# Optimization experiments

Measured on AMD Instinct MI355X. Metric: run time of the kernel, lower is better.

The kernel has to match this reference:

```python
import jax, jax.numpy as jnp
import numpy as np

B, G, C = 16384, 7, 30  # batch, 7x7 grid, 2*5 box params + 20 classes


def setup_inputs() -> dict:
    key = jax.random.key(0)
    k1, k2 = jax.random.split(key)
    pred = jax.random.uniform(k1, (B, G, G, C), dtype=jnp.float32)
    labels = jax.random.uniform(k2, (B, G, G, C), dtype=jnp.float32)
    # channel 0 of labels is the object-presence indicator (==1 where a gt box exists)
    labels = labels.at[..., 0].set((labels[..., 0] > 0.7).astype(jnp.float32))
    return {"pred": pred, "labels": labels}


def _corners(box):
    # box channels: [conf, x, y, w, h]
    x, y, w, h = box[..., 1], box[..., 2], box[..., 3], box[..., 4]
    return x - 0.5 * w, x + 0.5 * w, y - 0.5 * h, y + 0.5 * h  # left,right,top,bottom


def _iou(b1, b2):
    l1, r1, t1, bt1 = _corners(b1)
    l2, r2, t2, bt2 = _corners(b2)
    in_h = jnp.minimum(bt1, bt2) - jnp.maximum(t1, t2)
    in_w = jnp.minimum(r1, r2) - jnp.maximum(l1, l2)
    inter = jnp.where((in_h < 0) | (in_w < 0), 0.0, in_h * in_w)
    area1 = (bt1 - t1) * (r1 - l1)
    area2 = (bt2 - t2) * (r2 - l2)
    return inter / (area1 + area2 - inter)


def reference(pred, labels):
    mask = labels[..., 0]                     # [B,7,7] object indicator (0/1)
    box1 = pred[..., 0:5]
    box2 = pred[..., 5:10]
    gt = labels[..., 0:5]
    iou1 = _iou(box1, gt)
    iou2 = _iou(box2, gt)
    best = iou1 >= iou2                       # responsible box per cell
    sel = jnp.where(best[..., None], box1, box2)
    iou_max = jnp.where(best, iou1, iou2)
    iou_min = jnp.where(best, iou2, iou1)
    center = 5.0 * ((sel[..., 1] - gt[..., 1]) ** 2 + (sel[..., 2] - gt[..., 2]) ** 2)
    wh = 5.0 * ((jnp.sqrt(sel[..., 3]) - jnp.sqrt(gt[..., 3])) ** 2
                + (jnp.sqrt(sel[..., 4]) - jnp.sqrt(gt[..., 4])) ** 2)
    cls = jnp.sum((pred[..., 10:] - labels[..., 10:]) ** 2, axis=-1)

    def msum(x):
        return jnp.sum(x * mask)

    # [center, wh, obj_conf, noobj_conf, classification]
    return jnp.stack([msum(center), msum(wh), msum(iou_max), msum(iou_min), msum(cls)])
```

## Files before the change

### kernel.cpp

```cpp
#include <hip/hip_runtime.h>

#define NCH 30
#define TPB 256

typedef float v4f __attribute__((ext_vector_type(4)));
typedef float v2f __attribute__((ext_vector_type(2)));

__device__ __forceinline__ float iou_f(float x1, float y1, float w1, float h1,
                                       float x2, float y2, float w2, float h2) {
    float l1 = x1 - 0.5f * w1, r1 = x1 + 0.5f * w1;
    float t1 = y1 - 0.5f * h1, b1 = y1 + 0.5f * h1;
    float l2 = x2 - 0.5f * w2, r2 = x2 + 0.5f * w2;
    float t2 = y2 - 0.5f * h2, b2 = y2 + 0.5f * h2;
    float in_h = fminf(b1, b2) - fmaxf(t1, t2);
    float in_w = fminf(r1, r2) - fmaxf(l1, l2);
    float inter = (in_h < 0.f || in_w < 0.f) ? 0.f : in_h * in_w;
    float a1 = (b1 - t1) * (r1 - l1);
    float a2 = (b2 - t2) * (r2 - l2);
    return inter / (a1 + a2 - inter);
}

#define PF(i) (P[(i) >> 2][(i) & 3])
#define LF(i) (L[(i) >> 2][(i) & 3])

__device__ __forceinline__ void cell_terms(const v4f* P, const v4f* L, int o, float mask,
                                           float& v0, float& v1, float& v2,
                                           float& v3, float& v4) {
    const float gx = LF(o + 1), gy = LF(o + 2), gw = LF(o + 3), gh = LF(o + 4);
    const float i1 = iou_f(PF(o + 1), PF(o + 2), PF(o + 3), PF(o + 4), gx, gy, gw, gh);
    const float i2 = iou_f(PF(o + 6), PF(o + 7), PF(o + 8), PF(o + 9), gx, gy, gw, gh);
    const bool best = (i1 >= i2);
    const float sx = best ? PF(o + 1) : PF(o + 6);
    const float sy = best ? PF(o + 2) : PF(o + 7);
    const float sw = best ? PF(o + 3) : PF(o + 8);
    const float sh = best ? PF(o + 4) : PF(o + 9);
    const float imax = best ? i1 : i2;
    const float imin = best ? i2 : i1;

    const float center = 5.f * ((sx - gx) * (sx - gx) + (sy - gy) * (sy - gy));
    const float dw = sqrtf(sw) - sqrtf(gw);
    const float dh = sqrtf(sh) - sqrtf(gh);
    const float wh = 5.f * (dw * dw + dh * dh);

    float cls = 0.f;
#pragma unroll
    for (int c = 10; c < 30; ++c) {
        const float d = PF(o + c) - LF(o + c);
        cls += d * d;
    }

    v0 += center * mask;
    v1 += wh * mask;
    v2 += imax * mask;
    v3 += imin * mask;
    v4 += cls * mask;
}

__global__ __launch_bounds__(TPB) void yolo_partial(const float* __restrict__ pred,
                                                    const float* __restrict__ lab,
                                                    float* __restrict__ partial,
                                                    int n_pairs) {
    __shared__ float red[5][TPB / 64];
    const int tid = threadIdx.x;
    const size_t p = (size_t)blockIdx.x * TPB + tid;

    float v0 = 0.f, v1 = 0.f, v2 = 0.f, v3 = 0.f, v4 = 0.f;

    if (p < (size_t)n_pairs) {
        const float* lp = lab + p * (2 * NCH);
        const v2f mA = *(const v2f*)(lp);
        const v2f mB = *(const v2f*)(lp + NCH);
        const float maskA = mA[0], maskB = mB[0];

        if (maskA != 0.f || maskB != 0.f) {
            const float* pp = pred + p * (2 * NCH);
            v4f P[15], L[15];
#pragma unroll
            for (int k = 0; k < 15; ++k) P[k] = *(const v4f*)(pp + 4 * k);
#pragma unroll
            for (int k = 0; k < 15; ++k) L[k] = *(const v4f*)(lp + 4 * k);

            if (maskA != 0.f) cell_terms(P, L, 0,   maskA, v0, v1, v2, v3, v4);
            if (maskB != 0.f) cell_terms(P, L, NCH, maskB, v0, v1, v2, v3, v4);
        }
    }

#pragma unroll
    for (int off = 32; off > 0; off >>= 1) {
        v0 += __shfl_down(v0, off);
        v1 += __shfl_down(v1, off);
        v2 += __shfl_down(v2, off);
        v3 += __shfl_down(v3, off);
        v4 += __shfl_down(v4, off);
    }

    const int wave = tid >> 6;
    const int lane = tid & 63;
    if (lane == 0) {
        red[0][wave] = v0;
        red[1][wave] = v1;
        red[2][wave] = v2;
        red[3][wave] = v3;
        red[4][wave] = v4;
    }
    __syncthreads();

    if (tid < 5) {
        float s = 0.f;
#pragma unroll
        for (int w = 0; w < TPB / 64; ++w) s += red[tid][w];
        partial[(size_t)blockIdx.x * 5 + tid] = s;
    }
}

__global__ __launch_bounds__(256) void final_reduce(const float* __restrict__ partial,
                                                    float* __restrict__ out,
                                                    int n_blocks) {
    __shared__ float red[5][4];
    const int tid = threadIdx.x;
    float v0 = 0.f, v1 = 0.f, v2 = 0.f, v3 = 0.f, v4 = 0.f;
    for (int b = tid; b < n_blocks; b += 256) {
        const float* q = partial + (size_t)b * 5;
        v0 += q[0]; v1 += q[1]; v2 += q[2]; v3 += q[3]; v4 += q[4];
    }
#pragma unroll
    for (int off = 32; off > 0; off >>= 1) {
        v0 += __shfl_down(v0, off);
        v1 += __shfl_down(v1, off);
        v2 += __shfl_down(v2, off);
        v3 += __shfl_down(v3, off);
        v4 += __shfl_down(v4, off);
    }
    const int wave = tid >> 6;
    const int lane = tid & 63;
    if (lane == 0) {
        red[0][wave] = v0;
        red[1][wave] = v1;
        red[2][wave] = v2;
        red[3][wave] = v3;
        red[4][wave] = v4;
    }
    __syncthreads();
    if (tid < 5) {
        float s = 0.f;
#pragma unroll
        for (int w = 0; w < 4; ++w) s += red[tid][w];
        out[tid] = s;
    }
}

extern "C" void kernel_launch(void* const* d_in, const int* in_sizes, int n_in,
                              void* d_out, int out_size, void* d_ws, size_t ws_size,
                              hipStream_t stream) {
    const float* pred = (const float*)d_in[0];
    const float* lab  = (const float*)d_in[1];
    float* out = (float*)d_out;
    float* partial = (float*)d_ws;

    const int n_cells = in_sizes[0] / NCH;
    const int n_pairs = n_cells / 2;
    const int grid = (n_pairs + TPB - 1) / TPB;

    hipLaunchKernelGGL(yolo_partial, dim3(grid), dim3(TPB), 0, stream,
                       pred, lab, partial, n_pairs);
    hipLaunchKernelGGL(final_reduce, dim3(1), dim3(256), 0, stream,
                       partial, out, grid);
}
```

Baseline: 205.5 us.

## Stage 64-cell chunks into LDS via global_load_lds with persistent waves

Before, each thread read its own two cells with strided 16-byte vector loads, which coalesces poorly. Now each wave copies a contiguous 64-cell chunk of pred and labels into its own LDS buffer using direct global-to-LDS loads. Each lane then computes one cell from LDS, and a fixed grid of 512 blocks loops over the chunks grid-stride. The goal is fully coalesced memory traffic; in exchange, pred is now read even where both masks are zero. Each chunk is also waited on with vmcnt(0) with no double buffering, and the large LDS footprint limits how many blocks fit per CU.

```diff
diff --git a/kernel.cpp b/kernel.cpp
--- a/kernel.cpp
+++ b/kernel.cpp
@@ -1,10 +1,13 @@
 #include <hip/hip_runtime.h>
 
 #define NCH 30
+#define W   64
 #define TPB 256
+#define NV  (W * NCH / 4)
+#define NBLK 512
 
-typedef float v4f __attribute__((ext_vector_type(4)));
-typedef float v2f __attribute__((ext_vector_type(2)));
+typedef __attribute__((address_space(1))) const void gas_t;
+typedef __attribute__((address_space(3))) void las_t;
 
 __device__ __forceinline__ float iou_f(float x1, float y1, float w1, float h1,
                                        float x2, float y2, float w2, float h2) {
@@ -20,69 +23,74 @@
     return inter / (a1 + a2 - inter);
 }
 
-#define PF(i) (P[(i) >> 2][(i) & 3])
-#define LF(i) (L[(i) >> 2][(i) & 3])
-
-__device__ __forceinline__ void cell_terms(const v4f* P, const v4f* L, int o, float mask,
-                                           float& v0, float& v1, float& v2,
-                                           float& v3, float& v4) {
-    const float gx = LF(o + 1), gy = LF(o + 2), gw = LF(o + 3), gh = LF(o + 4);
-    const float i1 = iou_f(PF(o + 1), PF(o + 2), PF(o + 3), PF(o + 4), gx, gy, gw, gh);
-    const float i2 = iou_f(PF(o + 6), PF(o + 7), PF(o + 8), PF(o + 9), gx, gy, gw, gh);
-    const bool best = (i1 >= i2);
-    const float sx = best ? PF(o + 1) : PF(o + 6);
-    const float sy = best ? PF(o + 2) : PF(o + 7);
-    const float sw = best ? PF(o + 3) : PF(o + 8);
-    const float sh = best ? PF(o + 4) : PF(o + 9);
-    const float imax = best ? i1 : i2;
-    const float imin = best ? i2 : i1;
-
-    const float center = 5.f * ((sx - gx) * (sx - gx) + (sy - gy) * (sy - gy));
-    const float dw = sqrtf(sw) - sqrtf(gw);
-    const float dh = sqrtf(sh) - sqrtf(gh);
-    const float wh = 5.f * (dw * dw + dh * dh);
-
-    float cls = 0.f;
-#pragma unroll
-    for (int c = 10; c < 30; ++c) {
-        const float d = PF(o + c) - LF(o + c);
-        cls += d * d;
-    }
-
-    v0 += center * mask;
-    v1 += wh * mask;
-    v2 += imax * mask;
-    v3 += imin * mask;
-    v4 += cls * mask;
-}
-
 __global__ __launch_bounds__(TPB) void yolo_partial(const float* __restrict__ pred,
                                                     const float* __restrict__ lab,
                                                     float* __restrict__ partial,
-                                                    int n_pairs) {
-    __shared__ float red[5][TPB / 64];
-    const int tid = threadIdx.x;
-    const size_t p = (size_t)blockIdx.x * TPB + tid;
+                                                    int n_chunks, int total_waves) {
+    __shared__ float4 sbuf[4][2][NV];
+    __shared__ float red[5][4];
+
+    const int tid  = threadIdx.x;
+    const int wave = tid >> 6;
+    const int lane = tid & 63;
+    const int wid  = blockIdx.x * 4 + wave;
+
+    float4* sp = sbuf[wave][0];
+    float4* sl = sbuf[wave][1];
 
     float v0 = 0.f, v1 = 0.f, v2 = 0.f, v3 = 0.f, v4 = 0.f;
 
-    if (p < (size_t)n_pairs) {
-        const float* lp = lab + p * (2 * NCH);
-        const v2f mA = *(const v2f*)(lp);
-        const v2f mB = *(const v2f*)(lp + NCH);
-        const float maskA = mA[0], maskB = mB[0];
+    for (int ch = wid; ch < n_chunks; ch += total_waves) {
+        const float4* gp = (const float4*)pred + (size_t)ch * NV;
+        const float4* gl = (const float4*)lab  + (size_t)ch * NV;
 
-        if (maskA != 0.f || maskB != 0.f) {
-            const float* pp = pred + p * (2 * NCH);
-            v4f P[15], L[15];
 #pragma unroll
-            for (int k = 0; k < 15; ++k) P[k] = *(const v4f*)(pp + 4 * k);
+        for (int k = 0; k < 7; ++k) {
+            __builtin_amdgcn_global_load_lds((gas_t*)(gp + 64 * k + lane),
+                                             (las_t*)(sp + 64 * k), 16, 0, 0);
+            __builtin_amdgcn_global_load_lds((gas_t*)(gl + 64 * k + lane),
+                                             (las_t*)(sl + 64 * k), 16, 0, 0);
+        }
+        if (lane < 32) {
+            __builtin_amdgcn_global_load_lds((gas_t*)(gp + 448 + lane),
+                                             (las_t*)(sp + 448), 16, 0, 0);
+            __builtin_amdgcn_global_load_lds((gas_t*)(gl + 448 + lane),
+                                             (las_t*)(sl + 448), 16, 0, 0);
+        }
+        asm volatile("s_waitcnt vmcnt(0)" ::: "memory");
+
+        const float* cp = (const float*)sp + lane * NCH;
+        const float* cl = (const float*)sl + lane * NCH;
+        const float mask = cl[0];
+        const float gx = cl[1], gy = cl[2], gw = cl[3], gh = cl[4];
+
+        const float i1 = iou_f(cp[1], cp[2], cp[3], cp[4], gx, gy, gw, gh);
+        const float i2 = iou_f(cp[6], cp[7], cp[8], cp[9], gx, gy, gw, gh);
+        const bool best = (i1 >= i2);
+        const float sx = best ? cp[1] : cp[6];
+        const float sy = best ? cp[2] : cp[7];
+        const float sw = best ? cp[3] : cp[8];
+        const float sh = best ? cp[4] : cp[9];
+        const float imax = best ? i1 : i2;
+        const float imin = best ? i2 : i1;
+
+        const float center = 5.f * ((sx - gx) * (sx - gx) + (sy - gy) * (sy - gy));
+        const float dw = sqrtf(sw) - sqrtf(gw);
+        const float dh = sqrtf(sh) - sqrtf(gh);
+        const float wh = 5.f * (dw * dw + dh * dh);
+
+        float cls = 0.f;
 #pragma unroll
-            for (int k = 0; k < 15; ++k) L[k] = *(const v4f*)(lp + 4 * k);
+        for (int c = 10; c < 30; ++c) {
+            const float d = cp[c] - cl[c];
+            cls += d * d;
+        }
 
-            if (maskA != 0.f) cell_terms(P, L, 0,   maskA, v0, v1, v2, v3, v4);
-            if (maskB != 0.f) cell_terms(P, L, NCH, maskB, v0, v1, v2, v3, v4);
-        }
+        v0 += center * mask;
+        v1 += wh * mask;
+        v2 += imax * mask;
+        v3 += imin * mask;
+        v4 += cls * mask;
     }
 
 #pragma unroll
@@ -94,8 +102,6 @@
         v4 += __shfl_down(v4, off);
     }
 
-    const int wave = tid >> 6;
-    const int lane = tid & 63;
     if (lane == 0) {
         red[0][wave] = v0;
         red[1][wave] = v1;
@@ -108,7 +114,7 @@
     if (tid < 5) {
         float s = 0.f;
 #pragma unroll
-        for (int w = 0; w < TPB / 64; ++w) s += red[tid][w];
+        for (int w = 0; w < 4; ++w) s += red[tid][w];
         partial[(size_t)blockIdx.x * 5 + tid] = s;
     }
 }
@@ -157,12 +163,12 @@
     float* out = (float*)d_out;
     float* partial = (float*)d_ws;
 
-    const int n_cells = in_sizes[0] / NCH;
-    const int n_pairs = n_cells / 2;
-    const int grid = (n_pairs + TPB - 1) / TPB;
+    const int n_cells  = in_sizes[0] / NCH;
+    const int n_chunks = n_cells / W;
+    const int total_waves = NBLK * (TPB / 64);
 
-    hipLaunchKernelGGL(yolo_partial, dim3(grid), dim3(TPB), 0, stream,
-                       pred, lab, partial, n_pairs);
+    hipLaunchKernelGGL(yolo_partial, dim3(NBLK), dim3(TPB), 0, stream,
+                       pred, lab, partial, n_chunks, total_waves);
     hipLaunchKernelGGL(final_reduce, dim3(1), dim3(256), 0, stream,
-                       partial, out, grid);
+                       partial, out, NBLK);
 }
```

Result: no change. 209.4 us (+1.9%).
